# Optimization experiments

Hardware: AMD Instinct MI355X
Metric: run time of the kernel (lower is better)

## Reference

```python
import jax, jax.numpy as jnp
import numpy as np

B, T, I, H = 128, 512, 512, 512


def setup_inputs() -> dict:
    key = jax.random.key(0)
    k1, k2, k3, k4, k5 = jax.random.split(key, 5)
    scale_x = 1.0 / np.sqrt(I)
    scale_h = 1.0 / np.sqrt(H)
    return {
        "x": jax.random.normal(k1, (B, T, I), dtype=jnp.float32),
        "h0": jax.random.normal(k2, (B, H), dtype=jnp.float32),
        "Wx": jax.random.normal(k3, (3 * H, I), dtype=jnp.float32) * scale_x,
        "bx": jax.random.normal(k4, (3 * H,), dtype=jnp.float32) * scale_x,
        "Wh": jax.random.normal(k5, (3 * H, H), dtype=jnp.float32) * scale_h,
    }


def reference(x, h0, Wx, bx, Wh):
    # Precompute input projections for all timesteps as one big GEMM:
    # [B,T,I] @ [I,3H] -> [B,T,3H]
    x_lin = jnp.einsum('bti,ki->btk', x, Wx) + bx
    x_lin_t = jnp.swapaxes(x_lin, 0, 1)  # [T,B,3H] time-major for scan

    def step(h, xl):
        h_lin = h @ Wh.T                          # [B,3H]
        x_z, x_r, x_n = jnp.split(xl, 3, axis=1)
        h_z, h_r, h_n = jnp.split(h_lin, 3, axis=1)
        z = jax.nn.sigmoid(x_z + h_z)
        r = jax.nn.sigmoid(x_r + h_r)
        n = jnp.tanh(x_n + r * h_n)
        h_new = (1.0 - z) * n + z * h
        return h_new, h_new

    h_final, ys = jax.lax.scan(step, h0, x_lin_t)  # ys: [T,B,H]
    y = jnp.swapaxes(ys, 0, 1)                      # [B,T,H]
    return (y, h_final)
```

## Files before the change

### kernel.cpp

```cpp
#include <hip/hip_runtime.h>
#include <hip/hip_bf16.h>

#define B_  128
#define T_  512
#define HID 512
#define NG  1536
#define CSTRIDE 16

#define GCNT(t)  ((t)*CSTRIDE)
#define FLAG0    (T_*CSTRIDE)
#define MEM0     (T_*CSTRIDE + T_*8*32)
#define INIT0    (MEM0 + 8*CSTRIDE)
#define SYNC_U32 (INIT0 + CSTRIDE)

typedef __attribute__((ext_vector_type(8))) short bf16x8;
typedef __attribute__((ext_vector_type(4))) float f32x4;
typedef unsigned int uint;

__device__ __forceinline__ float bf2f(unsigned short h) {
  union { unsigned u; float f; } c; c.u = ((unsigned)h) << 16; return c.f;
}
__device__ __forceinline__ unsigned short f2bf_rn(float f) {
  union { float f; unsigned u; } c; c.f = f;
  return (unsigned short)((c.u + 0x7FFFu + ((c.u >> 16) & 1u)) >> 16);
}
__device__ __forceinline__ void split1(float f, short& hi, short& lo) {
  union { float f; unsigned u; } c; c.f = f;
  unsigned short h = (unsigned short)(c.u >> 16);
  float r = f - bf2f(h);
  hi = (short)h; lo = (short)f2bf_rn(r);
}
__device__ __forceinline__ void split8(float4 a, float4 b, bf16x8& hi, bf16x8& lo) {
  float v[8] = {a.x,a.y,a.z,a.w,b.x,b.y,b.z,b.w};
  #pragma unroll
  for (int i = 0; i < 8; ++i) { short h,l; split1(v[i],h,l); hi[i]=h; lo[i]=l; }
}
__device__ __forceinline__ uint packh(float f) {
  short hi, lo; split1(f, hi, lo);
  return (((uint)(unsigned short)hi) << 16) | (uint)(unsigned short)lo;
}
__device__ __forceinline__ float unpackh(uint u) {
  return bf2f((unsigned short)(u >> 16)) + bf2f((unsigned short)(u & 0xFFFFu));
}

__device__ __forceinline__ uint aload_rlx(const uint* p) {
  return __hip_atomic_load(p, __ATOMIC_RELAXED, __HIP_MEMORY_SCOPE_AGENT);
}

__global__ void h0_pack(const float* __restrict__ h0, uint* __restrict__ hbuf) {
  int i = blockIdx.x * 256 + threadIdx.x;
  hbuf[65536 + i] = packh(h0[i]);
}

template<bool WSF32>
__global__ __launch_bounds__(256) void xlin_kernel(const float* __restrict__ x,
                                                   const float* __restrict__ Wx,
                                                   const float* __restrict__ bx,
                                                   void* __restrict__ xlin) {
  const int lane = threadIdx.x & 63;
  const int w    = threadIdx.x >> 6;
  const int wm   = w & 1, wn = w >> 1;
  const int quad = lane >> 4, l16 = lane & 15;
  const long m0  = (long)blockIdx.y * 128;
  const int  n0  = blockIdx.x * 128;

  f32x4 acc[4][4];
  #pragma unroll
  for (int i = 0; i < 4; ++i)
    #pragma unroll
    for (int j = 0; j < 4; ++j) acc[i][j] = (f32x4){0.f,0.f,0.f,0.f};

  for (int kk = 0; kk < 16; ++kk) {
    const int kq = kk*32 + quad*8;
    bf16x8 ahi[4], alo[4], bhi[4], blo[4];
    #pragma unroll
    for (int i = 0; i < 4; ++i) {
      const float* p = x + (m0 + wm*64 + i*16 + l16) * HID + kq;
      float4 f0 = ((const float4*)p)[0], f1 = ((const float4*)p)[1];
      split8(f0, f1, ahi[i], alo[i]);
      const float* q = Wx + (long)(n0 + wn*64 + i*16 + l16) * HID + kq;
      float4 g0 = ((const float4*)q)[0], g1 = ((const float4*)q)[1];
      split8(g0, g1, bhi[i], blo[i]);
    }
    #pragma unroll
    for (int i = 0; i < 4; ++i)
      #pragma unroll
      for (int j = 0; j < 4; ++j) {
        acc[i][j] = __builtin_amdgcn_mfma_f32_16x16x32_bf16(ahi[i], bhi[j], acc[i][j], 0, 0, 0);
        acc[i][j] = __builtin_amdgcn_mfma_f32_16x16x32_bf16(ahi[i], blo[j], acc[i][j], 0, 0, 0);
        acc[i][j] = __builtin_amdgcn_mfma_f32_16x16x32_bf16(alo[i], bhi[j], acc[i][j], 0, 0, 0);
      }
  }
  #pragma unroll
  for (int i = 0; i < 4; ++i) {
    #pragma unroll
    for (int j = 0; j < 4; ++j) {
      const int n = n0 + wn*64 + j*16 + l16;
      const float bias = bx[n];
      #pragma unroll
      for (int r = 0; r < 4; ++r) {
        const long m = m0 + wm*64 + i*16 + quad*4 + r;
        const float v = acc[i][j][r] + bias;
        if (WSF32) ((float*)xlin)[m * NG + n] = v;
        else       ((unsigned short*)xlin)[m * NG + n] = f2bf_rn(v);
      }
    }
  }
}

template<bool WSF32>
__global__ __launch_bounds__(256, 1) void gru_rec(const void* __restrict__ xlin,
                                                  const float* __restrict__ Wh,
                                                  uint* __restrict__ hbuf,
                                                  uint* __restrict__ sync,
                                                  float* __restrict__ out) {
  __shared__ float red[3][4][16][17];
  __shared__ int sh_xcd, sh_cb, sh_kc;
  __shared__ uint sh_fast;
  const int tid  = threadIdx.x;
  const int lane = tid & 63;
  const int w    = tid >> 6;
  const int quad = lane >> 4, l16 = lane & 15;

  if (tid == 0) {
    uint id;
    __asm__ volatile("s_getreg_b32 %0, hwreg(HW_REG_XCC_ID, 0, 32)" : "=s"(id));
    const int xcd = (int)(id & 7u);
    uint xr = __hip_atomic_fetch_add(&sync[MEM0 + xcd*CSTRIDE], 1u,
                                     __ATOMIC_RELAXED, __HIP_MEMORY_SCOPE_AGENT);
    uint* ic = &sync[INIT0];
    uint gr = __hip_atomic_fetch_add(ic, 1u, __ATOMIC_ACQ_REL, __HIP_MEMORY_SCOPE_AGENT);
    while (aload_rlx(ic) < 256u) __builtin_amdgcn_s_sleep(1);
    (void)__hip_atomic_load(ic, __ATOMIC_ACQUIRE, __HIP_MEMORY_SCOPE_AGENT);
    bool bal = true;
    #pragma unroll
    for (int x = 0; x < 8; ++x)
      bal = bal && (aload_rlx(&sync[MEM0 + x*CSTRIDE]) == 32u);
    sh_xcd  = xcd;
    sh_fast = bal ? 1u : 0u;
    sh_cb   = bal ? xcd     : (int)(gr >> 5);
    sh_kc   = bal ? (int)xr : (int)(gr & 31u);
  }
  __syncthreads();
  const int  xcd   = sh_xcd;
  const bool fastm = (sh_fast != 0u);
  const int  cb    = sh_cb;
  const int  kc    = sh_kc;

  bf16x8 Bhi[3][4], Blo[3][4];
  #pragma unroll
  for (int g = 0; g < 3; ++g)
    #pragma unroll
    for (int kk = 0; kk < 4; ++kk) {
      const float* p = Wh + (long)(g*HID + kc*16 + l16) * HID + w*128 + kk*32 + quad*8;
      float4 f0 = ((const float4*)p)[0], f1 = ((const float4*)p)[1];
      split8(f0, f1, Bhi[g][kk], Blo[g][kk]);
    }

  const int bb   = tid >> 4;
  const int kk_  = tid & 15;
  const int brow = cb*16 + bb;
  const int ncol = kc*16 + kk_;
  float* yout = out;
  float* hfin = out + (long)B_ * T_ * HID;

  uint* const hb0 = hbuf;
  uint* const hb1 = hbuf + 65536;

  for (int t = 0; t < T_; ++t) {
    float xz, xr, xn;
    {
      const long mrow = (long)brow * T_ + t;
      if (WSF32) {
        const float* xp = (const float*)xlin + mrow * NG + ncol;
        xz = xp[0]; xr = xp[HID]; xn = xp[2*HID];
      } else {
        const unsigned short* xp = (const unsigned short*)xlin + mrow * NG + ncol;
        xz = bf2f(xp[0]); xr = bf2f(xp[HID]); xn = bf2f(xp[2*HID]);
      }
    }

    if (t > 0) {
      if (fastm) {
        const uint* fp = &sync[FLAG0 + (((t-1)*8 + xcd) << 5) + (lane & 31)];
        while (!__all(aload_rlx(fp) != 0u)) __builtin_amdgcn_s_sleep(1);
      } else {
        if (tid == 0) {
          uint* gp = &sync[GCNT(t-1)];
          while (aload_rlx(gp) < 256u) __builtin_amdgcn_s_sleep(1);
          (void)__hip_atomic_load(gp, __ATOMIC_ACQUIRE, __HIP_MEMORY_SCOPE_AGENT);
        }
        __syncthreads();
      }
    }

    const uint* rb = ((t + 1) & 1) ? hb1 : hb0;
    uint*       wb = (t & 1)       ? hb1 : hb0;

    const uint* hp_ = rb + (cb*16 + l16)*HID + w*128 + quad*8;
    uint4 u0,u1,u2,u3,u4,u5,u6,u7;
    asm volatile(
      "global_load_dwordx4 %0, %8, off sc0\n\t"
      "global_load_dwordx4 %1, %8, off offset:16 sc0\n\t"
      "global_load_dwordx4 %2, %8, off offset:128 sc0\n\t"
      "global_load_dwordx4 %3, %8, off offset:144 sc0\n\t"
      "global_load_dwordx4 %4, %8, off offset:256 sc0\n\t"
      "global_load_dwordx4 %5, %8, off offset:272 sc0\n\t"
      "global_load_dwordx4 %6, %8, off offset:384 sc0\n\t"
      "global_load_dwordx4 %7, %8, off offset:400 sc0\n\t"
      "s_waitcnt vmcnt(0)"
      : "=&v"(u0), "=&v"(u1), "=&v"(u2), "=&v"(u3),
        "=&v"(u4), "=&v"(u5), "=&v"(u6), "=&v"(u7)
      : "v"(hp_)
      : "memory");
    const uint hpu = __hip_atomic_load(rb + brow*HID + ncol,
                                       __ATOMIC_RELAXED, __HIP_MEMORY_SCOPE_AGENT);

    const uint4 uu[4][2] = {{u0,u1},{u2,u3},{u4,u5},{u6,u7}};
    f32x4 acc[3] = { (f32x4){0,0,0,0}, (f32x4){0,0,0,0}, (f32x4){0,0,0,0} };
    #pragma unroll
    for (int kk = 0; kk < 4; ++kk) {
      bf16x8 ah, al;
      #pragma unroll
      for (int i = 0; i < 4; ++i) {
        uint v0 = ((const uint*)&uu[kk][0])[i];
        uint v1 = ((const uint*)&uu[kk][1])[i];
        ah[i]   = (short)(v0 >> 16); al[i]   = (short)(v0 & 0xFFFFu);
        ah[i+4] = (short)(v1 >> 16); al[i+4] = (short)(v1 & 0xFFFFu);
      }
      #pragma unroll
      for (int g = 0; g < 3; ++g) {
        acc[g] = __builtin_amdgcn_mfma_f32_16x16x32_bf16(ah, Bhi[g][kk], acc[g], 0, 0, 0);
        acc[g] = __builtin_amdgcn_mfma_f32_16x16x32_bf16(ah, Blo[g][kk], acc[g], 0, 0, 0);
        acc[g] = __builtin_amdgcn_mfma_f32_16x16x32_bf16(al, Bhi[g][kk], acc[g], 0, 0, 0);
      }
    }
    #pragma unroll
    for (int g = 0; g < 3; ++g)
      #pragma unroll
      for (int r = 0; r < 4; ++r)
        red[g][w][quad*4 + r][l16] = acc[g][r];

    const float hp = unpackh(hpu);

    __syncthreads();

    float az = 0.f, ar = 0.f, an = 0.f;
    #pragma unroll
    for (int ww = 0; ww < 4; ++ww) {
      az += red[0][ww][bb][kk_];
      ar += red[1][ww][bb][kk_];
      an += red[2][ww][bb][kk_];
    }
    const float z = 1.f / (1.f + __expf(-(az + xz)));
    const float r = 1.f / (1.f + __expf(-(ar + xr)));
    const float pre = xn + r * an;
    const float e2 = __expf(-2.f * pre);
    const float n = 2.f / (1.f + e2) - 1.f;
    const float hn = (1.f - z) * n + z * hp;

    if (t < T_ - 1) {
      wb[brow*HID + ncol] = packh(hn);
    } else {
      hfin[brow*HID + ncol] = hn;
    }

    __syncthreads();
    if (t < T_ - 1) {
      if (fastm) {
        if (tid == 0) sync[FLAG0 + ((t*8 + xcd) << 5) + kc] = 1u;
      } else {
        if (tid == 0)
          __hip_atomic_fetch_add(&sync[GCNT(t)], 1u,
                                 __ATOMIC_RELEASE, __HIP_MEMORY_SCOPE_AGENT);
      }
    }

    __builtin_nontemporal_store(hn, &yout[((long)brow * T_ + t) * HID + ncol]);
  }
}

extern "C" void kernel_launch(void* const* d_in, const int* in_sizes, int n_in,
                              void* d_out, int out_size, void* d_ws, size_t ws_size,
                              hipStream_t stream) {
  const float* x  = (const float*)d_in[0];
  const float* h0 = (const float*)d_in[1];
  const float* Wx = (const float*)d_in[2];
  const float* bx = (const float*)d_in[3];
  const float* Wh = (const float*)d_in[4];
  float* out = (float*)d_out;

  const size_t xlin_f32  = (size_t)B_ * T_ * NG * 4;
  const size_t xlin_bf16 = (size_t)B_ * T_ * NG * 2;
  const size_t hbuf_sz   = (size_t)2 * 65536 * 4;
  const size_t sync_sz   = (size_t)SYNC_U32 * 4;

  const bool wsf32 = (ws_size >= xlin_f32 + hbuf_sz + sync_sz);
  const size_t xsz = wsf32 ? xlin_f32 : xlin_bf16;
  void* xlin = d_ws;
  uint* hbuf = (uint*)((char*)d_ws + xsz);
  uint* sync = (uint*)((char*)d_ws + xsz + hbuf_sz);

  hipMemsetAsync(sync, 0, sync_sz, stream);
  h0_pack<<<256, 256, 0, stream>>>(h0, hbuf);
  if (wsf32) {
    xlin_kernel<true ><<<dim3(12, 512), 256, 0, stream>>>(x, Wx, bx, xlin);
    gru_rec<true >    <<<256, 256, 0, stream>>>(xlin, Wh, hbuf, sync, out);
  } else {
    xlin_kernel<false><<<dim3(12, 512), 256, 0, stream>>>(x, Wx, bx, xlin);
    gru_rec<false>    <<<256, 256, 0, stream>>>(xlin, Wh, hbuf, sync, out);
  }
}
```

Measured before the change: 2.134 ms.

## Split hidden state into hi/lo bf16 planes, batch x prefetch and y stores, monotonic flags

```diff
diff --git a/kernel.cpp b/kernel.cpp
--- a/kernel.cpp
+++ b/kernel.cpp
@@ -9,13 +9,17 @@
 
 #define GCNT(t)  ((t)*CSTRIDE)
 #define FLAG0    (T_*CSTRIDE)
-#define MEM0     (T_*CSTRIDE + T_*8*32)
+#define MEM0     (FLAG0 + 256*CSTRIDE)
 #define INIT0    (MEM0 + 8*CSTRIDE)
 #define SYNC_U32 (INIT0 + CSTRIDE)
 
 typedef __attribute__((ext_vector_type(8))) short bf16x8;
 typedef __attribute__((ext_vector_type(4))) float f32x4;
 typedef unsigned int uint;
+typedef unsigned short u16;
+
+#define HROW 1024
+#define HPAR 131072
 
 __device__ __forceinline__ float bf2f(unsigned short h) {
   union { unsigned u; float f; } c; c.u = ((unsigned)h) << 16; return c.f;
@@ -35,21 +39,17 @@
   #pragma unroll
   for (int i = 0; i < 8; ++i) { short h,l; split1(v[i],h,l); hi[i]=h; lo[i]=l; }
 }
-__device__ __forceinline__ uint packh(float f) {
-  short hi, lo; split1(f, hi, lo);
-  return (((uint)(unsigned short)hi) << 16) | (uint)(unsigned short)lo;
-}
-__device__ __forceinline__ float unpackh(uint u) {
-  return bf2f((unsigned short)(u >> 16)) + bf2f((unsigned short)(u & 0xFFFFu));
-}
 
 __device__ __forceinline__ uint aload_rlx(const uint* p) {
   return __hip_atomic_load(p, __ATOMIC_RELAXED, __HIP_MEMORY_SCOPE_AGENT);
 }
 
-__global__ void h0_pack(const float* __restrict__ h0, uint* __restrict__ hbuf) {
+__global__ void h0_pack(const float* __restrict__ h0, u16* __restrict__ hbuf) {
   int i = blockIdx.x * 256 + threadIdx.x;
-  hbuf[65536 + i] = packh(h0[i]);
+  short hi, lo; split1(h0[i], hi, lo);
+  u16* p = hbuf + HPAR + (i >> 9) * HROW + (i & 511);
+  p[0]   = (u16)hi;
+  p[512] = (u16)lo;
 }
 
 template<bool WSF32>
@@ -111,7 +111,7 @@
 template<bool WSF32>
 __global__ __launch_bounds__(256, 1) void gru_rec(const void* __restrict__ xlin,
                                                   const float* __restrict__ Wh,
-                                                  uint* __restrict__ hbuf,
+                                                  u16* __restrict__ hbuf,
                                                   uint* __restrict__ sync,
                                                   float* __restrict__ out) {
   __shared__ float red[3][4][16][17];
@@ -164,119 +164,154 @@
   float* yout = out;
   float* hfin = out + (long)B_ * T_ * HID;
 
-  uint* const hb0 = hbuf;
-  uint* const hb1 = hbuf + 65536;
-
-  for (int t = 0; t < T_; ++t) {
-    float xz, xr, xn;
-    {
-      const long mrow = (long)brow * T_ + t;
+  const int fragoff = (cb*16 + l16)*HROW + w*128 + quad*8;
+  const int hpoff   = brow*HROW + ncol;
+
+  float xq[8][3];
+  float yq[8];
+
+  {
+    const long base = (long)brow * T_;
+    #pragma unroll
+    for (int q = 0; q < 8; ++q) {
       if (WSF32) {
-        const float* xp = (const float*)xlin + mrow * NG + ncol;
-        xz = xp[0]; xr = xp[HID]; xn = xp[2*HID];
+        const float* xp = (const float*)xlin + (base + q) * NG + ncol;
+        xq[q][0] = xp[0]; xq[q][1] = xp[HID]; xq[q][2] = xp[2*HID];
       } else {
-        const unsigned short* xp = (const unsigned short*)xlin + mrow * NG + ncol;
-        xz = bf2f(xp[0]); xr = bf2f(xp[HID]); xn = bf2f(xp[2*HID]);
-      }
-    }
-
-    if (t > 0) {
-      if (fastm) {
-        const uint* fp = &sync[FLAG0 + (((t-1)*8 + xcd) << 5) + (lane & 31)];
-        while (!__all(aload_rlx(fp) != 0u)) __builtin_amdgcn_s_sleep(1);
+        const unsigned short* xp = (const unsigned short*)xlin + (base + q) * NG + ncol;
+        xq[q][0] = bf2f(xp[0]); xq[q][1] = bf2f(xp[HID]); xq[q][2] = bf2f(xp[2*HID]);
+      }
+    }
+  }
+
+  for (int tb = 0; tb < T_/8; ++tb) {
+    #pragma unroll
+    for (int ts = 0; ts < 8; ++ts) {
+      const int t = tb*8 + ts;
+      const float xz = xq[ts][0], xr = xq[ts][1], xn = xq[ts][2];
+
+      if (t > 0) {
+        if (fastm) {
+          const uint* fp = &sync[FLAG0 + (xcd*32 + (lane & 31))*CSTRIDE];
+          while (!__all(aload_rlx(fp) >= (uint)t)) __builtin_amdgcn_s_sleep(1);
+        } else {
+          if (tid == 0) {
+            uint* gp = &sync[GCNT(t-1)];
+            while (aload_rlx(gp) < 256u) __builtin_amdgcn_s_sleep(1);
+            (void)__hip_atomic_load(gp, __ATOMIC_ACQUIRE, __HIP_MEMORY_SCOPE_AGENT);
+          }
+          __syncthreads();
+        }
+      }
+
+      const u16* rb = hbuf + ((t + 1) & 1) * HPAR;
+      u16*       wb = hbuf + (t & 1)       * HPAR;
+
+      const u16* hp_ = rb + fragoff;
+      const u16* hpp = rb + hpoff;
+      uint4 u0,u1,u2,u3,u4,u5,u6,u7; uint hu, lu;
+      asm volatile(
+        "global_load_dwordx4 %0, %10, off sc0\n\t"
+        "global_load_dwordx4 %1, %10, off offset:64 sc0\n\t"
+        "global_load_dwordx4 %2, %10, off offset:128 sc0\n\t"
+        "global_load_dwordx4 %3, %10, off offset:192 sc0\n\t"
+        "global_load_dwordx4 %4, %10, off offset:1024 sc0\n\t"
+        "global_load_dwordx4 %5, %10, off offset:1088 sc0\n\t"
+        "global_load_dwordx4 %6, %10, off offset:1152 sc0\n\t"
+        "global_load_dwordx4 %7, %10, off offset:1216 sc0\n\t"
+        "global_load_ushort %8, %11, off sc0\n\t"
+        "global_load_ushort %9, %11, off offset:1024 sc0\n\t"
+        "s_waitcnt vmcnt(0)"
+        : "=&v"(u0), "=&v"(u1), "=&v"(u2), "=&v"(u3),
+          "=&v"(u4), "=&v"(u5), "=&v"(u6), "=&v"(u7),
+          "=&v"(hu), "=&v"(lu)
+        : "v"(hp_), "v"(hpp)
+        : "memory");
+
+      f32x4 acc[3] = { (f32x4){0,0,0,0}, (f32x4){0,0,0,0}, (f32x4){0,0,0,0} };
+      {
+        const bf16x8 ah0 = *(const bf16x8*)&u0, al0 = *(const bf16x8*)&u4;
+        const bf16x8 ah1 = *(const bf16x8*)&u1, al1 = *(const bf16x8*)&u5;
+        const bf16x8 ah2 = *(const bf16x8*)&u2, al2 = *(const bf16x8*)&u6;
+        const bf16x8 ah3 = *(const bf16x8*)&u3, al3 = *(const bf16x8*)&u7;
+        const bf16x8 AH[4] = {ah0, ah1, ah2, ah3};
+        const bf16x8 AL[4] = {al0, al1, al2, al3};
+        #pragma unroll
+        for (int kk = 0; kk < 4; ++kk) {
+          #pragma unroll
+          for (int g = 0; g < 3; ++g) {
+            acc[g] = __builtin_amdgcn_mfma_f32_16x16x32_bf16(AH[kk], Bhi[g][kk], acc[g], 0, 0, 0);
+            acc[g] = __builtin_amdgcn_mfma_f32_16x16x32_bf16(AH[kk], Blo[g][kk], acc[g], 0, 0, 0);
+            acc[g] = __builtin_amdgcn_mfma_f32_16x16x32_bf16(AL[kk], Bhi[g][kk], acc[g], 0, 0, 0);
+          }
+        }
+      }
+      #pragma unroll
+      for (int g = 0; g < 3; ++g)
+        #pragma unroll
+        for (int r = 0; r < 4; ++r)
+          red[g][w][quad*4 + r][l16] = acc[g][r];
+
+      const float hp = bf2f((unsigned short)hu) + bf2f((unsigned short)lu);
+
+      __syncthreads();
+
+      float az = 0.f, ar = 0.f, an = 0.f;
+      #pragma unroll
+      for (int ww = 0; ww < 4; ++ww) {
+        az += red[0][ww][bb][kk_];
+        ar += red[1][ww][bb][kk_];
+        an += red[2][ww][bb][kk_];
+      }
+      const float z = 1.f / (1.f + __expf(-(az + xz)));
+      const float r = 1.f / (1.f + __expf(-(ar + xr)));
+      const float pre = xn + r * an;
+      const float e2 = __expf(-2.f * pre);
+      const float n = 2.f / (1.f + e2) - 1.f;
+      const float hn = (1.f - z) * n + z * hp;
+      yq[ts] = hn;
+
+      if (t < T_ - 1) {
+        short shi, slo; split1(hn, shi, slo);
+        u16* wp = wb + hpoff;
+        wp[0]   = (u16)shi;
+        wp[512] = (u16)slo;
       } else {
-        if (tid == 0) {
-          uint* gp = &sync[GCNT(t-1)];
-          while (aload_rlx(gp) < 256u) __builtin_amdgcn_s_sleep(1);
-          (void)__hip_atomic_load(gp, __ATOMIC_ACQUIRE, __HIP_MEMORY_SCOPE_AGENT);
+        hfin[brow*HID + ncol] = hn;
+      }
+
+      __syncthreads();
+      if (t < T_ - 1) {
+        if (fastm) {
+          if (tid == 0)
+            sync[FLAG0 + (xcd*32 + kc)*CSTRIDE] = (uint)(t + 1);
+        } else {
+          if (tid == 0)
+            __hip_atomic_fetch_add(&sync[GCNT(t)], 1u,
+                                   __ATOMIC_RELEASE, __HIP_MEMORY_SCOPE_AGENT);
         }
-        __syncthreads();
-      }
-    }
-
-    const uint* rb = ((t + 1) & 1) ? hb1 : hb0;
-    uint*       wb = (t & 1)       ? hb1 : hb0;
-
-    const uint* hp_ = rb + (cb*16 + l16)*HID + w*128 + quad*8;
-    uint4 u0,u1,u2,u3,u4,u5,u6,u7;
-    asm volatile(
-      "global_load_dwordx4 %0, %8, off sc0\n\t"
-      "global_load_dwordx4 %1, %8, off offset:16 sc0\n\t"
-      "global_load_dwordx4 %2, %8, off offset:128 sc0\n\t"
-      "global_load_dwordx4 %3, %8, off offset:144 sc0\n\t"
-      "global_load_dwordx4 %4, %8, off offset:256 sc0\n\t"
-      "global_load_dwordx4 %5, %8, off offset:272 sc0\n\t"
-      "global_load_dwordx4 %6, %8, off offset:384 sc0\n\t"
-      "global_load_dwordx4 %7, %8, off offset:400 sc0\n\t"
-      "s_waitcnt vmcnt(0)"
-      : "=&v"(u0), "=&v"(u1), "=&v"(u2), "=&v"(u3),
-        "=&v"(u4), "=&v"(u5), "=&v"(u6), "=&v"(u7)
-      : "v"(hp_)
-      : "memory");
-    const uint hpu = __hip_atomic_load(rb + brow*HID + ncol,
-                                       __ATOMIC_RELAXED, __HIP_MEMORY_SCOPE_AGENT);
-
-    const uint4 uu[4][2] = {{u0,u1},{u2,u3},{u4,u5},{u6,u7}};
-    f32x4 acc[3] = { (f32x4){0,0,0,0}, (f32x4){0,0,0,0}, (f32x4){0,0,0,0} };
-    #pragma unroll
-    for (int kk = 0; kk < 4; ++kk) {
-      bf16x8 ah, al;
-      #pragma unroll
-      for (int i = 0; i < 4; ++i) {
-        uint v0 = ((const uint*)&uu[kk][0])[i];
-        uint v1 = ((const uint*)&uu[kk][1])[i];
-        ah[i]   = (short)(v0 >> 16); al[i]   = (short)(v0 & 0xFFFFu);
-        ah[i+4] = (short)(v1 >> 16); al[i+4] = (short)(v1 & 0xFFFFu);
-      }
-      #pragma unroll
-      for (int g = 0; g < 3; ++g) {
-        acc[g] = __builtin_amdgcn_mfma_f32_16x16x32_bf16(ah, Bhi[g][kk], acc[g], 0, 0, 0);
-        acc[g] = __builtin_amdgcn_mfma_f32_16x16x32_bf16(ah, Blo[g][kk], acc[g], 0, 0, 0);
-        acc[g] = __builtin_amdgcn_mfma_f32_16x16x32_bf16(al, Bhi[g][kk], acc[g], 0, 0, 0);
-      }
-    }
-    #pragma unroll
-    for (int g = 0; g < 3; ++g)
-      #pragma unroll
-      for (int r = 0; r < 4; ++r)
-        red[g][w][quad*4 + r][l16] = acc[g][r];
-
-    const float hp = unpackh(hpu);
-
-    __syncthreads();
-
-    float az = 0.f, ar = 0.f, an = 0.f;
-    #pragma unroll
-    for (int ww = 0; ww < 4; ++ww) {
-      az += red[0][ww][bb][kk_];
-      ar += red[1][ww][bb][kk_];
-      an += red[2][ww][bb][kk_];
-    }
-    const float z = 1.f / (1.f + __expf(-(az + xz)));
-    const float r = 1.f / (1.f + __expf(-(ar + xr)));
-    const float pre = xn + r * an;
-    const float e2 = __expf(-2.f * pre);
-    const float n = 2.f / (1.f + e2) - 1.f;
-    const float hn = (1.f - z) * n + z * hp;
-
-    if (t < T_ - 1) {
-      wb[brow*HID + ncol] = packh(hn);
-    } else {
-      hfin[brow*HID + ncol] = hn;
-    }
-
-    __syncthreads();
-    if (t < T_ - 1) {
-      if (fastm) {
-        if (tid == 0) sync[FLAG0 + ((t*8 + xcd) << 5) + kc] = 1u;
-      } else {
-        if (tid == 0)
-          __hip_atomic_fetch_add(&sync[GCNT(t)], 1u,
-                                 __ATOMIC_RELEASE, __HIP_MEMORY_SCOPE_AGENT);
-      }
-    }
-
-    __builtin_nontemporal_store(hn, &yout[((long)brow * T_ + t) * HID + ncol]);
+      }
+
+      if (ts == 7) {
+        #pragma unroll
+        for (int q = 0; q < 8; ++q)
+          __builtin_nontemporal_store(yq[q],
+              &yout[((long)brow * T_ + tb*8 + q) * HID + ncol]);
+        if (tb + 1 < T_/8) {
+          const long base = (long)brow * T_ + (tb + 1)*8;
+          #pragma unroll
+          for (int q = 0; q < 8; ++q) {
+            if (WSF32) {
+              const float* xp = (const float*)xlin + (base + q) * NG + ncol;
+              xq[q][0] = xp[0]; xq[q][1] = xp[HID]; xq[q][2] = xp[2*HID];
+            } else {
+              const unsigned short* xp = (const unsigned short*)xlin + (base + q) * NG + ncol;
+              xq[q][0] = bf2f(xp[0]); xq[q][1] = bf2f(xp[HID]); xq[q][2] = bf2f(xp[2*HID]);
+            }
+          }
+        }
+      }
+    }
   }
 }
 
@@ -292,13 +327,13 @@
 
   const size_t xlin_f32  = (size_t)B_ * T_ * NG * 4;
   const size_t xlin_bf16 = (size_t)B_ * T_ * NG * 2;
-  const size_t hbuf_sz   = (size_t)2 * 65536 * 4;
+  const size_t hbuf_sz   = (size_t)2 * HPAR * 2;
   const size_t sync_sz   = (size_t)SYNC_U32 * 4;
 
   const bool wsf32 = (ws_size >= xlin_f32 + hbuf_sz + sync_sz);
   const size_t xsz = wsf32 ? xlin_f32 : xlin_bf16;
   void* xlin = d_ws;
-  uint* hbuf = (uint*)((char*)d_ws + xsz);
+  u16*  hbuf = (u16*)((char*)d_ws + xsz);
   uint* sync = (uint*)((char*)d_ws + xsz + hbuf_sz);
 
   hipMemsetAsync(sync, 0, sync_sz, stream);
```

Result: faster. 2.022 ms (-5.2%).
